# Kernel tuning notes

Measured on AMD Instinct MI355X. Metric: run time of the kernel, lower is better.

The kernel has to match this reference:

```python
import jax, jax.numpy as jnp
import numpy as np

HEADS = 4
DIM_QK = 128
SCALE = DIM_QK ** (-0.5)


def rel_to_abs(x):
    # x: [B, Nh, L, 2L-1] -> [B, Nh, L, L] via the skew trick
    B, Nh, L, _ = x.shape
    x = jnp.pad(x, ((0, 0), (0, 0), (0, 0), (0, 1)))          # [B,Nh,L,2L]
    flat = x.reshape(B, Nh, L * 2 * L)
    flat = jnp.pad(flat, ((0, 0), (0, 0), (0, L - 1)))
    final = flat.reshape(B, Nh, L + 1, 2 * L - 1)
    return final[:, :, :L, L - 1:]


def relative_logits_1d(q, rel_k):
    # q: [B, Nh, H, W, d], rel_k: [2W-1, d] -> [B, Nh, H, H, W, W] (axes b h x i y j)
    B, Nh, H, W, _ = q.shape
    rl = jnp.einsum('bnhwd,md->bnhwm', q, rel_k)              # [B,Nh,H,W,2W-1]
    rl = rl.reshape(B, Nh * H, W, 2 * W - 1)
    rl = rel_to_abs(rl)                                        # [B,Nh*H,W,W]
    rl = rl.reshape(B, Nh, H, W, W)
    rl = jnp.broadcast_to(rl[:, :, :, None, :, :], (B, Nh, H, H, W, W))
    return rl


def rel_pos_logits(q, rel_height, rel_width, H, W):
    # q: [B, h, HW, d]
    B, h, L, d = q.shape
    qg = q.reshape(B, h, H, W, d)
    # width direction: b h x i y j -> b h (x y) (i j)
    rw = relative_logits_1d(qg, rel_width)                     # [B,h,H,H,W,W]
    rw = rw.transpose(0, 1, 2, 4, 3, 5).reshape(B, h, H * W, H * W)
    # height direction: transpose x<->y, then b h x i y j -> b h (y x) (j i)
    qh = qg.transpose(0, 1, 3, 2, 4)                           # [B,h,W,H,d]
    rh = relative_logits_1d(qh, rel_height)                    # [B,h,W,W,H,H]
    rh = rh.transpose(0, 1, 4, 2, 5, 3).reshape(B, h, H * W, H * W)
    return rw + rh


def setup_inputs() -> dict:
    key = jax.random.key(0)
    ks = jax.random.split(key, 5)
    B, C, H, W = 16, 512, 32, 32
    scale = DIM_QK ** (-0.5)
    return {
        'featuremap': jax.random.normal(ks[0], (B, C, H, W), jnp.float32),
        'w_qk': jax.random.normal(ks[1], (2 * HEADS * DIM_QK, C), jnp.float32) * (C ** -0.5),
        'w_v': jax.random.normal(ks[2], (HEADS * 128, C), jnp.float32) * (C ** -0.5),
        'rel_height': jax.random.normal(ks[3], (2 * H - 1, DIM_QK), jnp.float32) * scale,
        'rel_width': jax.random.normal(ks[4], (2 * W - 1, DIM_QK), jnp.float32) * scale,
    }


def reference(featuremap, w_qk, w_v, rel_height, rel_width):
    B, C, H, W = featuremap.shape
    L = H * W
    # 1x1 conv projections (no bias) == channel matmuls
    qk = jnp.einsum('bchw,oc->bohw', featuremap, w_qk)         # [B, 2*h*dqk, H, W]
    v = jnp.einsum('bchw,oc->bohw', featuremap, w_v)           # [B, h*dv, H, W]
    q, k = jnp.split(qk, 2, axis=1)

    def to_heads(x):
        # B (h d) H W -> B h (H W) d
        d = x.shape[1] // HEADS
        return x.reshape(B, HEADS, d, L).transpose(0, 1, 3, 2)

    q, k, v = to_heads(q), to_heads(k), to_heads(v)
    q = q * SCALE
    logits = jnp.einsum('bhxd,bhyd->bhxy', q, k)
    logits = logits + rel_pos_logits(q, rel_height, rel_width, H, W)
    weights = jax.nn.softmax(logits, axis=-1)
    attn_out = jnp.einsum('bhxy,bhyd->bhxd', weights, v)       # [B,h,L,dv]
    dv = attn_out.shape[-1]
    # B h (H W) d -> B (h d) H W
    return attn_out.transpose(0, 1, 3, 2).reshape(B, HEADS * dv, H, W)
```

## Files before the change

kernel.cpp:

```cpp
#include <hip/hip_runtime.h>
#include <stdint.h>

typedef __attribute__((ext_vector_type(4))) float f32x4;
typedef __attribute__((ext_vector_type(8))) short bf16x8;

#define DEV static __device__ __forceinline__

#define GLOAD16(g, l) __builtin_amdgcn_global_load_lds( \
    (const __attribute__((address_space(1))) void*)(g), \
    (__attribute__((address_space(3))) void*)(l), 16, 0, 0)

DEV unsigned short f2bf(float f){
  union { float f; uint32_t u; } v; v.f = f;
  return (unsigned short)((v.u + 0x7fffu + ((v.u >> 16) & 1u)) >> 16);
}

DEV f32x4 mfma_bf16(bf16x8 a, bf16x8 b, f32x4 c){
  return __builtin_amdgcn_mfma_f32_16x16x32_bf16(a, b, c, 0, 0, 0);
}

__global__ __launch_bounds__(256) void k_transpose_cvt(const float* __restrict__ fm,
                                                       unsigned short* __restrict__ xt){
  __shared__ float tile[32][33];
  int b = blockIdx.z, c0 = blockIdx.y * 32, l0 = blockIdx.x * 32;
  int tc = threadIdx.x & 31, tr = threadIdx.x >> 5;
  const float* src = fm + ((size_t)b * 512 + c0) * 1024 + l0;
  for (int i = 0; i < 4; i++){
    int r = tr + i * 8;
    tile[r][tc] = src[(size_t)r * 1024 + tc];
  }
  __syncthreads();
  unsigned short* dst = xt + ((size_t)b * 1024 + l0) * 512 + c0;
  for (int i = 0; i < 4; i++){
    int r = tr + i * 8;
    dst[(size_t)r * 512 + tc] = f2bf(tile[tc][r]);
  }
}

__global__ __launch_bounds__(256) void k_wcvt(const float* __restrict__ wqk,
                                              const float* __restrict__ wv,
                                              unsigned short* __restrict__ wb){
  int idx = blockIdx.x * 256 + threadIdx.x;
  int e = idx * 4;
  if (e >= 1536 * 512) return;
  const float* src = (e < 1024 * 512) ? (wqk + e) : (wv + (e - 1024 * 512));
  f32x4 v = *(const f32x4*)src;
  unsigned short* d = wb + e;
  d[0] = f2bf(v[0]); d[1] = f2bf(v[1]); d[2] = f2bf(v[2]); d[3] = f2bf(v[3]);
}

template<int MODE>
__global__ __launch_bounds__(256, 3) void k_proj(const unsigned short* __restrict__ Abase,
                                                 const unsigned short* __restrict__ Bbase,
                                                 unsigned short* __restrict__ qbuf,
                                                 unsigned short* __restrict__ kbuf,
                                                 unsigned short* __restrict__ vbuf){
  __shared__ unsigned short Al[128][64];
  __shared__ unsigned short Bl[128][64];
  int b = blockIdx.z;
  const unsigned short* A = Abase + (MODE == 0 ? (size_t)b * 1024 * 512 : 0);
  const unsigned short* B = Bbase + (MODE == 0 ? 0 : (size_t)b * 1024 * 512);
  int m0 = blockIdx.x * 128, n0 = blockIdx.y * 128;
  int t = threadIdx.x;
  int lane = t & 63, w = t >> 6;
  int wm = (w >> 1) * 64, wn = (w & 1) * 64;
  int l15 = lane & 15, lg = lane >> 4;
  int srow = lane >> 3;
  int scol = (lane & 7) * 8;
  f32x4 acc[4][4];
  for (int m = 0; m < 4; m++) for (int n = 0; n < 4; n++) acc[m][n] = (f32x4)(0.f);
  for (int k0 = 0; k0 < 512; k0 += 64){
    __syncthreads();
    #pragma unroll
    for (int i = 0; i < 4; i++){
      int j = w * 4 + i;
      GLOAD16(&A[(size_t)(m0 + j * 8 + srow) * 512 + k0 + scol], &Al[j * 8][0]);
      GLOAD16(&B[(size_t)(n0 + j * 8 + srow) * 512 + k0 + scol], &Bl[j * 8][0]);
    }
    __syncthreads();
    for (int dc = 0; dc < 2; dc++){
      bf16x8 af[4], bfr[4];
      for (int m = 0; m < 4; m++) af[m]  = *(const bf16x8*)&Al[wm + m * 16 + l15][dc * 32 + lg * 8];
      for (int n = 0; n < 4; n++) bfr[n] = *(const bf16x8*)&Bl[wn + n * 16 + l15][dc * 32 + lg * 8];
      for (int m = 0; m < 4; m++)
        for (int n = 0; n < 4; n++)
          acc[m][n] = mfma_bf16(af[m], bfr[n], acc[m][n]);
    }
  }
  for (int m = 0; m < 4; m++) for (int n = 0; n < 4; n++) for (int r = 0; r < 4; r++){
    int row = m0 + wm + m * 16 + lg * 4 + r;
    int col = n0 + wn + n * 16 + l15;
    float val = acc[m][n][r];
    if (MODE == 0){
      if (col < 512){
        int h = col >> 7, d = col & 127;
        qbuf[(((size_t)b * 4 + h) * 1024 + row) * 128 + d] = f2bf(val * 0.08838834764831845f);
      } else {
        int c2 = col - 512;
        int h = c2 >> 7, d = c2 & 127;
        kbuf[(((size_t)b * 4 + h) * 1024 + row) * 128 + d] = f2bf(val);
      }
    } else {
      vbuf[(((size_t)b * 4 + (row >> 7)) * 128 + (row & 127)) * 1024 + col] = f2bf(val);
    }
  }
}

__global__ __launch_bounds__(64, 4) void k_rel(const unsigned short* __restrict__ qbuf,
                                               const float* __restrict__ relh,
                                               const float* __restrict__ relw,
                                               float* __restrict__ Rel){
  int xi = blockIdx.x;
  int bh = blockIdx.y;
  int mode = blockIdx.z;
  int lane = threadIdx.x;
  int l15 = lane & 15, lg = lane >> 4;
  const float* rel = (mode == 0) ? relh : relw;
  f32x4 acc[2][2];
  for (int m = 0; m < 2; m++) for (int n = 0; n < 2; n++) acc[m][n] = (f32x4)(0.f);
  for (int dc = 0; dc < 4; dc++){
    bf16x8 af[2], bb[2];
    for (int m = 0; m < 2; m++){
      int p = (mode == 0) ? (xi * 32 + m * 16 + l15) : ((m * 16 + l15) * 32 + xi);
      af[m] = *(const bf16x8*)&qbuf[((size_t)bh * 1024 + p) * 128 + dc * 32 + lg * 8];
    }
    for (int n = 0; n < 2; n++){
      int mrow = n * 16 + l15 - xi + 31;
      const float* rp = &rel[(size_t)mrow * 128 + dc * 32 + lg * 8];
      f32x4 r0 = *(const f32x4*)rp;
      f32x4 r1 = *(const f32x4*)(rp + 4);
      bf16x8 tt;
      for (int e = 0; e < 4; e++){ tt[e] = (short)f2bf(r0[e]); tt[e + 4] = (short)f2bf(r1[e]); }
      bb[n] = tt;
    }
    for (int m = 0; m < 2; m++)
      for (int n = 0; n < 2; n++)
        acc[m][n] = mfma_bf16(af[m], bb[n], acc[m][n]);
  }
  for (int m = 0; m < 2; m++) for (int n = 0; n < 2; n++) for (int r = 0; r < 4; r++){
    int a = m * 16 + lg * 4 + r;
    int outc = n * 16 + l15;
    int p = (mode == 0) ? (xi * 32 + a) : (a * 32 + xi);
    Rel[((size_t)bh * 1024 + p) * 64 + ((mode == 0) ? outc : 32 + outc)] = acc[m][n][r];
  }
}

__global__ __launch_bounds__(256, 2) void k_attn(const unsigned short* __restrict__ qbuf,
                                                 const unsigned short* __restrict__ kbuf,
                                                 const unsigned short* __restrict__ vbuf,
                                                 const float* __restrict__ Rel,
                                                 float* __restrict__ out){
  __shared__ unsigned short Kl[64][136];
  __shared__ unsigned short Vl[128][72];
  __shared__ unsigned short Pl[4][32][72];
  int bh = blockIdx.x;
  int q0 = blockIdx.y * 128;
  int t = threadIdx.x;
  int lane = t & 63, w = t >> 6;
  int l15 = lane & 15, lg = lane >> 4;
  int qw = q0 + w * 32;
  const unsigned short* qg = qbuf + (size_t)bh * 1024 * 128;
  const unsigned short* kg = kbuf + (size_t)bh * 1024 * 128;
  const unsigned short* vg = vbuf + (size_t)bh * 128 * 1024;
  const float* relbh = Rel + (size_t)bh * 1024 * 64;

  bf16x8 qf[2][4];
  for (int cg = 0; cg < 2; cg++)
    for (int dc = 0; dc < 4; dc++)
      qf[cg][dc] = *(const bf16x8*)&qg[(size_t)(qw + cg * 16 + l15) * 128 + dc * 32 + lg * 8];

  float rw[2][2][4];
  for (int cg = 0; cg < 2; cg++)
    for (int kk = 0; kk < 2; kk++)
      for (int r = 0; r < 4; r++)
        rw[cg][kk][r] = relbh[(size_t)(qw + cg * 16 + l15) * 64 + 32 + kk * 16 + lg * 4 + r];

  int krow = (t + 0) >> 4;
  (void)krow;
  f32x4 o[8][2];
  for (int rg = 0; rg < 8; rg++) for (int cg = 0; cg < 2; cg++) o[rg][cg] = (f32x4)(0.f);
  float mrun[2] = {-1e30f, -1e30f};
  float lrun[2] = {0.f, 0.f};

  bf16x8 kpre[4], vpre[4];
  #pragma unroll
  for (int i = 0; i < 4; i++){
    int c = t + i * 256;
    kpre[i] = *(const bf16x8*)&kg[(size_t)(c >> 4) * 128 + (c & 15) * 8];
    vpre[i] = *(const bf16x8*)&vg[(size_t)(c >> 3) * 1024 + 0 + (c & 7) * 8];
  }

  for (int kv0 = 0; kv0 < 1024; kv0 += 64){
    __syncthreads();
    #pragma unroll
    for (int i = 0; i < 4; i++){
      int c = t + i * 256;
      *(bf16x8*)&Kl[c >> 4][(c & 15) * 8] = kpre[i];
      *(bf16x8*)&Vl[c >> 3][(c & 7) * 8] = vpre[i];
    }
    __syncthreads();
    if (kv0 + 64 < 1024){
      int kvn = kv0 + 64;
      #pragma unroll
      for (int i = 0; i < 4; i++){
        int c = t + i * 256;
        kpre[i] = *(const bf16x8*)&kg[(size_t)(kvn + (c >> 4)) * 128 + (c & 15) * 8];
        vpre[i] = *(const bf16x8*)&vg[(size_t)(c >> 3) * 1024 + kvn + (c & 7) * 8];
      }
    }

    f32x4 s[4][2];
    for (int g = 0; g < 4; g++) for (int cg = 0; cg < 2; cg++) s[g][cg] = (f32x4)(0.f);
    for (int dc = 0; dc < 4; dc++){
      bf16x8 kf[4];
      for (int g = 0; g < 4; g++)
        kf[g] = *(const bf16x8*)&Kl[g * 16 + l15][dc * 32 + lg * 8];
      for (int g = 0; g < 4; g++)
        for (int cg = 0; cg < 2; cg++)
          s[g][cg] = mfma_bf16(kf[g], qf[cg][dc], s[g][cg]);
    }
    int y0 = kv0 >> 5;
    float rh[2][2];
    for (int cg = 0; cg < 2; cg++){
      const float* rp = &relbh[(size_t)(qw + cg * 16 + l15) * 64];
      rh[cg][0] = rp[y0];
      rh[cg][1] = rp[y0 + 1];
    }
    for (int g = 0; g < 4; g++)
      for (int cg = 0; cg < 2; cg++)
        for (int r = 0; r < 4; r++)
          s[g][cg][r] += rh[cg][g >> 1] + rw[cg][g & 1][r];

    float mt[2];
    for (int cg = 0; cg < 2; cg++){
      float m_ = s[0][cg][0];
      for (int g = 0; g < 4; g++) for (int r = 0; r < 4; r++) m_ = fmaxf(m_, s[g][cg][r]);
      m_ = fmaxf(m_, __shfl_xor(m_, 16, 64));
      m_ = fmaxf(m_, __shfl_xor(m_, 32, 64));
      mt[cg] = m_;
    }
    bool defer = (mt[0] <= mrun[0] + 8.f) && (mt[1] <= mrun[1] + 8.f);
    if (!__all((int)defer)){
      for (int cg = 0; cg < 2; cg++){
        float mnew = fmaxf(mrun[cg], mt[cg]);
        float a_ = __expf(mrun[cg] - mnew);
        mrun[cg] = mnew;
        lrun[cg] *= a_;
        for (int rg = 0; rg < 8; rg++){
          o[rg][cg][0] *= a_; o[rg][cg][1] *= a_;
          o[rg][cg][2] *= a_; o[rg][cg][3] *= a_;
        }
      }
    }
    for (int cg = 0; cg < 2; cg++){
      float sum = 0.f;
      for (int g = 0; g < 4; g++) for (int r = 0; r < 4; r++){
        float e = __expf(s[g][cg][r] - mrun[cg]);
        s[g][cg][r] = e;
        sum += e;
      }
      sum += __shfl_xor(sum, 16, 64);
      sum += __shfl_xor(sum, 32, 64);
      lrun[cg] += sum;
    }
    for (int cg = 0; cg < 2; cg++)
      for (int g = 0; g < 4; g++){
        uint32_t p0 = (uint32_t)f2bf(s[g][cg][0]) | ((uint32_t)f2bf(s[g][cg][1]) << 16);
        uint32_t p1 = (uint32_t)f2bf(s[g][cg][2]) | ((uint32_t)f2bf(s[g][cg][3]) << 16);
        uint2 pv = make_uint2(p0, p1);
        *(uint2*)&Pl[w][cg * 16 + l15][g * 16 + lg * 4] = pv;
      }
    for (int kc = 0; kc < 2; kc++){
      bf16x8 pf[2];
      for (int cg = 0; cg < 2; cg++)
        pf[cg] = *(const bf16x8*)&Pl[w][cg * 16 + l15][kc * 32 + lg * 8];
      for (int rg = 0; rg < 8; rg++){
        bf16x8 vf = *(const bf16x8*)&Vl[rg * 16 + l15][kc * 32 + lg * 8];
        for (int cg = 0; cg < 2; cg++)
          o[rg][cg] = mfma_bf16(vf, pf[cg], o[rg][cg]);
      }
    }
  }
  float inv[2] = {1.f / lrun[0], 1.f / lrun[1]};
  float* outb = out + (size_t)bh * 128 * 1024;
  for (int rg = 0; rg < 8; rg++)
    for (int cg = 0; cg < 2; cg++)
      for (int r = 0; r < 4; r++){
        int dv = rg * 16 + lg * 4 + r;
        int p = qw + cg * 16 + l15;
        outb[(size_t)dv * 1024 + p] = o[rg][cg][r] * inv[cg];
      }
}

extern "C" void kernel_launch(void* const* d_in, const int* in_sizes, int n_in,
                              void* d_out, int out_size, void* d_ws, size_t ws_size,
                              hipStream_t stream){
  const float* fm   = (const float*)d_in[0];
  const float* wqk  = (const float*)d_in[1];
  const float* wv   = (const float*)d_in[2];
  const float* relh = (const float*)d_in[3];
  const float* relw = (const float*)d_in[4];
  float* out = (float*)d_out;
  char* ws = (char*)d_ws;
  if (ws_size < (size_t)68681728) return;

  unsigned short* qb = (unsigned short*)(ws);
  unsigned short* kb = (unsigned short*)(ws + ((size_t)16 << 20));
  unsigned short* vb = (unsigned short*)(ws + ((size_t)32 << 20));
  unsigned short* xt = (unsigned short*)(ws + ((size_t)48 << 20));
  float* Rel         = (float*)(ws + ((size_t)48 << 20));
  unsigned short* wb = (unsigned short*)(ws + ((size_t)64 << 20));

  hipLaunchKernelGGL(k_transpose_cvt, dim3(32, 16, 16), dim3(256), 0, stream, fm, xt);
  hipLaunchKernelGGL(k_wcvt, dim3(768), dim3(256), 0, stream, wqk, wv, wb);
  hipLaunchKernelGGL(k_proj<0>, dim3(8, 8, 16), dim3(256), 0, stream, xt, wb, qb, kb, vb);
  hipLaunchKernelGGL(k_proj<1>, dim3(4, 8, 16), dim3(256), 0, stream,
                     wb + (size_t)1024 * 512, xt, qb, kb, vb);
  hipLaunchKernelGGL(k_rel, dim3(32, 64, 2), dim3(64), 0, stream, qb, relh, relw, Rel);
  hipLaunchKernelGGL(k_attn, dim3(64, 8), dim3(256), 0, stream, qb, kb, vb, Rel, out);
}
```

Measured before the change: 130.5 us.

## Swizzle attention LDS tiles, vectorize transpose, use packed bf16 convert and setprio

Replaces the padded LDS arrays in the attention kernel with XOR-swizzled layouts for K, V and P, aiming to avoid bank conflicts while saving LDS. The transpose kernel now uses 64x64 tiles with vectorized float4 loads and 16-byte bf16 stores, launched on a smaller grid. P conversion uses the hardware packed bf16 convert instruction, and s_setprio is raised around the MFMA loops. The swizzle has to match on every read and write, and the packed convert's rounding may differ slightly from the manual rounding.

```diff
diff --git a/kernel.cpp b/kernel.cpp
--- a/kernel.cpp
+++ b/kernel.cpp
@@ -15,25 +15,40 @@
   return (unsigned short)((v.u + 0x7fffu + ((v.u >> 16) & 1u)) >> 16);
 }
 
+DEV uint32_t cvtpk(float a, float b){
+  uint32_t r; asm("v_cvt_pk_bf16_f32 %0, %1, %2" : "=v"(r) : "v"(a), "v"(b)); return r;
+}
+
 DEV f32x4 mfma_bf16(bf16x8 a, bf16x8 b, f32x4 c){
   return __builtin_amdgcn_mfma_f32_16x16x32_bf16(a, b, c, 0, 0, 0);
 }
 
 __global__ __launch_bounds__(256) void k_transpose_cvt(const float* __restrict__ fm,
                                                        unsigned short* __restrict__ xt){
-  __shared__ float tile[32][33];
-  int b = blockIdx.z, c0 = blockIdx.y * 32, l0 = blockIdx.x * 32;
-  int tc = threadIdx.x & 31, tr = threadIdx.x >> 5;
+  __shared__ float tile[64][65];
+  int b = blockIdx.z, c0 = blockIdx.y * 64, l0 = blockIdx.x * 64;
+  int t = threadIdx.x;
+  int lr = t >> 4;
+  int lc4 = (t & 15) * 4;
   const float* src = fm + ((size_t)b * 512 + c0) * 1024 + l0;
+  #pragma unroll
   for (int i = 0; i < 4; i++){
-    int r = tr + i * 8;
-    tile[r][tc] = src[(size_t)r * 1024 + tc];
+    int r = lr + i * 16;
+    f32x4 v = *(const f32x4*)&src[(size_t)r * 1024 + lc4];
+    tile[r][lc4] = v[0]; tile[r][lc4 + 1] = v[1];
+    tile[r][lc4 + 2] = v[2]; tile[r][lc4 + 3] = v[3];
   }
   __syncthreads();
+  int j = t & 7;
+  int lrow = t >> 3;
   unsigned short* dst = xt + ((size_t)b * 1024 + l0) * 512 + c0;
-  for (int i = 0; i < 4; i++){
-    int r = tr + i * 8;
-    dst[(size_t)r * 512 + tc] = f2bf(tile[tc][r]);
+  #pragma unroll
+  for (int i = 0; i < 2; i++){
+    int l = lrow + i * 32;
+    unsigned short tmp[8];
+    #pragma unroll
+    for (int u = 0; u < 8; u++) tmp[u] = f2bf(tile[j * 8 + u][l]);
+    *(uint4*)&dst[(size_t)l * 512 + j * 8] = *(const uint4*)tmp;
   }
 }
 
@@ -150,14 +165,15 @@
                                                  const unsigned short* __restrict__ vbuf,
                                                  const float* __restrict__ Rel,
                                                  float* __restrict__ out){
-  __shared__ unsigned short Kl[64][136];
-  __shared__ unsigned short Vl[128][72];
-  __shared__ unsigned short Pl[4][32][72];
+  __shared__ unsigned short Kl[64 * 128];
+  __shared__ unsigned short Vl[128 * 64];
+  __shared__ unsigned short Pl[4][32 * 64];
   int bh = blockIdx.x;
   int q0 = blockIdx.y * 128;
   int t = threadIdx.x;
   int lane = t & 63, w = t >> 6;
   int l15 = lane & 15, lg = lane >> 4;
+  int swz = (l15 & 7) * 8;
   int qw = q0 + w * 32;
   const unsigned short* qg = qbuf + (size_t)bh * 1024 * 128;
   const unsigned short* kg = kbuf + (size_t)bh * 1024 * 128;
@@ -175,8 +191,6 @@
       for (int r = 0; r < 4; r++)
         rw[cg][kk][r] = relbh[(size_t)(qw + cg * 16 + l15) * 64 + 32 + kk * 16 + lg * 4 + r];
 
-  int krow = (t + 0) >> 4;
-  (void)krow;
   f32x4 o[8][2];
   for (int rg = 0; rg < 8; rg++) for (int cg = 0; cg < 2; cg++) o[rg][cg] = (f32x4)(0.f);
   float mrun[2] = {-1e30f, -1e30f};
@@ -187,7 +201,7 @@
   for (int i = 0; i < 4; i++){
     int c = t + i * 256;
     kpre[i] = *(const bf16x8*)&kg[(size_t)(c >> 4) * 128 + (c & 15) * 8];
-    vpre[i] = *(const bf16x8*)&vg[(size_t)(c >> 3) * 1024 + 0 + (c & 7) * 8];
+    vpre[i] = *(const bf16x8*)&vg[(size_t)(c >> 3) * 1024 + (c & 7) * 8];
   }
 
   for (int kv0 = 0; kv0 < 1024; kv0 += 64){
@@ -195,8 +209,10 @@
     #pragma unroll
     for (int i = 0; i < 4; i++){
       int c = t + i * 256;
-      *(bf16x8*)&Kl[c >> 4][(c & 15) * 8] = kpre[i];
-      *(bf16x8*)&Vl[c >> 3][(c & 7) * 8] = vpre[i];
+      int kr = c >> 4;
+      int vr = c >> 3;
+      *(bf16x8*)&Kl[kr * 128 + (((c & 15) * 8) ^ ((kr & 7) * 8))] = kpre[i];
+      *(bf16x8*)&Vl[vr * 64 + (((c & 7) * 8) ^ ((vr & 7) * 8))] = vpre[i];
     }
     __syncthreads();
     if (kv0 + 64 < 1024){
@@ -211,14 +227,17 @@
 
     f32x4 s[4][2];
     for (int g = 0; g < 4; g++) for (int cg = 0; cg < 2; cg++) s[g][cg] = (f32x4)(0.f);
+    __builtin_amdgcn_s_setprio(1);
     for (int dc = 0; dc < 4; dc++){
       bf16x8 kf[4];
       for (int g = 0; g < 4; g++)
-        kf[g] = *(const bf16x8*)&Kl[g * 16 + l15][dc * 32 + lg * 8];
+        kf[g] = *(const bf16x8*)&Kl[(g * 16 + l15) * 128 + ((dc * 32 + lg * 8) ^ swz)];
       for (int g = 0; g < 4; g++)
         for (int cg = 0; cg < 2; cg++)
           s[g][cg] = mfma_bf16(kf[g], qf[cg][dc], s[g][cg]);
     }
+    __builtin_amdgcn_s_setprio(0);
+
     int y0 = kv0 >> 5;
     float rh[2][2];
     for (int cg = 0; cg < 2; cg++){
@@ -246,10 +265,7 @@
         float a_ = __expf(mrun[cg] - mnew);
         mrun[cg] = mnew;
         lrun[cg] *= a_;
-        for (int rg = 0; rg < 8; rg++){
-          o[rg][cg][0] *= a_; o[rg][cg][1] *= a_;
-          o[rg][cg][2] *= a_; o[rg][cg][3] *= a_;
-        }
+        for (int rg = 0; rg < 8; rg++) o[rg][cg] *= a_;
       }
     }
     for (int cg = 0; cg < 2; cg++){
@@ -265,21 +281,22 @@
     }
     for (int cg = 0; cg < 2; cg++)
       for (int g = 0; g < 4; g++){
-        uint32_t p0 = (uint32_t)f2bf(s[g][cg][0]) | ((uint32_t)f2bf(s[g][cg][1]) << 16);
-        uint32_t p1 = (uint32_t)f2bf(s[g][cg][2]) | ((uint32_t)f2bf(s[g][cg][3]) << 16);
-        uint2 pv = make_uint2(p0, p1);
-        *(uint2*)&Pl[w][cg * 16 + l15][g * 16 + lg * 4] = pv;
-      }
+        uint2 pv = make_uint2(cvtpk(s[g][cg][0], s[g][cg][1]),
+                              cvtpk(s[g][cg][2], s[g][cg][3]));
+        *(uint2*)&Pl[w][(cg * 16 + l15) * 64 + ((g * 16 + lg * 4) ^ swz)] = pv;
+      }
+    __builtin_amdgcn_s_setprio(1);
     for (int kc = 0; kc < 2; kc++){
       bf16x8 pf[2];
       for (int cg = 0; cg < 2; cg++)
-        pf[cg] = *(const bf16x8*)&Pl[w][cg * 16 + l15][kc * 32 + lg * 8];
+        pf[cg] = *(const bf16x8*)&Pl[w][(cg * 16 + l15) * 64 + ((kc * 32 + lg * 8) ^ swz)];
       for (int rg = 0; rg < 8; rg++){
-        bf16x8 vf = *(const bf16x8*)&Vl[rg * 16 + l15][kc * 32 + lg * 8];
+        bf16x8 vf = *(const bf16x8*)&Vl[(rg * 16 + l15) * 64 + ((kc * 32 + lg * 8) ^ swz)];
         for (int cg = 0; cg < 2; cg++)
           o[rg][cg] = mfma_bf16(vf, pf[cg], o[rg][cg]);
       }
     }
+    __builtin_amdgcn_s_setprio(0);
   }
   float inv[2] = {1.f / lrun[0], 1.f / lrun[1]};
   float* outb = out + (size_t)bh * 128 * 1024;
@@ -311,7 +328,7 @@
   float* Rel         = (float*)(ws + ((size_t)48 << 20));
   unsigned short* wb = (unsigned short*)(ws + ((size_t)64 << 20));
 
-  hipLaunchKernelGGL(k_transpose_cvt, dim3(32, 16, 16), dim3(256), 0, stream, fm, xt);
+  hipLaunchKernelGGL(k_transpose_cvt, dim3(16, 8, 16), dim3(256), 0, stream, fm, xt);
   hipLaunchKernelGGL(k_wcvt, dim3(768), dim3(256), 0, stream, wqk, wv, wb);
   hipLaunchKernelGGL(k_proj<0>, dim3(8, 8, 16), dim3(256), 0, stream, xt, wb, qb, kb, vb);
   hipLaunchKernelGGL(k_proj<1>, dim3(4, 8, 16), dim3(256), 0, stream,
```

New measurement: 123.4 us. -5.5%, faster.
